# Performance work log

Measured on AMD Instinct MI355X. Metric: run time of the kernel, lower is better.

Reference implementation:

```python
import jax, jax.numpy as jnp
import numpy as np

B, F, D, OUT = 1024, 256, 256, 128
EXP = [10, 25]          # expansion_rates
CUM = [1, 10]           # cum_expansion_rates


def setup_inputs() -> dict:
    key = jax.random.key(0)
    ks = jax.random.split(key, 12)
    s = 0.05
    return {
        "h0": jax.random.normal(ks[0], (B, 1, F), jnp.float32),
        "h1": jax.random.normal(ks[1], (B, EXP[0], F), jnp.float32),
        "h2": jax.random.normal(ks[2], (B, EXP[0] * EXP[1], F), jnp.float32),
        "mask0": (jax.random.uniform(ks[3], (B, 1, EXP[0], 1)) < 0.9).astype(jnp.float32),
        "mask1": (jax.random.uniform(ks[4], (B, EXP[0], EXP[1], 1)) < 0.9).astype(jnp.float32),
        "W_self0": jax.random.normal(ks[5], (D, F), jnp.float32) * s,
        "W_neigh0": jax.random.normal(ks[6], (D, F), jnp.float32) * s,
        "W_pool0": jax.random.normal(ks[7], (D, D), jnp.float32) * s,
        "W_self1": jax.random.normal(ks[8], (D, 2 * D), jnp.float32) * s,
        "W_neigh1": jax.random.normal(ks[9], (D, 2 * D), jnp.float32) * s,
        "W_pool1": jax.random.normal(ks[10], (D, D), jnp.float32) * s,
        "W_out": jax.random.normal(ks[11], (OUT, 2 * D), jnp.float32) * s,
    }


def _sage_layer(x_self, x_neigh, mask, Ws, Wn, Wp):
    # x_self: (B, P, Fin), x_neigh: (B, P, S, Fin), mask: (B, P, S, 1)
    h_self = x_self @ Ws.T                                  # (B, P, D)
    h_neigh = jax.nn.relu(x_neigh @ Wn.T) * mask            # (B, P, S, D)
    h_pool = jnp.max(h_neigh, axis=-2) @ Wp.T               # (B, P, D) -- max pooling
    return jnp.concatenate([h_self, h_pool], axis=-1)       # (B, P, 2D)


def reference(h0, h1, h2, mask0, mask1,
              W_self0, W_neigh0, W_pool0,
              W_self1, W_neigh1, W_pool1, W_out):
    states = [h0, h1, h2]
    masks = [mask0, mask1]
    layers = [(W_self0, W_neigh0, W_pool0), (W_self1, W_neigh1, W_pool1)]
    layer_input_sizes = [F, 2 * D]
    depth = 2
    for i, (Ws, Wn, Wp) in enumerate(layers):
        fin = layer_input_sizes[i]
        for j in range(depth - i):
            x_self = states[j]
            x_neigh = states[j + 1].reshape(-1, CUM[j], EXP[j], fin)
            m = masks[j].reshape(-1, CUM[j], EXP[j], 1)
            states[j] = _sage_layer(x_self, x_neigh, m, Ws, Wn, Wp)
    return states[0][:, 0] @ W_out.T  # (B, OUT)
```

## Files before the change

### kernel.cpp

```cpp
#include <hip/hip_runtime.h>
#include <hip/hip_bf16.h>


typedef __bf16 bf16_t;
typedef bf16_t bf16x8 __attribute__((ext_vector_type(8)));
typedef float  f32x4  __attribute__((ext_vector_type(4)));

__device__ inline bf16x8 cvt8(const float4 a, const float4 b) {
  bf16x8 t;
  t[0]=(bf16_t)a.x; t[1]=(bf16_t)a.y; t[2]=(bf16_t)a.z; t[3]=(bf16_t)a.w;
  t[4]=(bf16_t)b.x; t[5]=(bf16_t)b.y; t[6]=(bf16_t)b.z; t[7]=(bf16_t)b.w;
  return t;
}

__global__ __launch_bounds__(256) void cvt_bf16(
    const float* __restrict__ s, bf16_t* __restrict__ d, int n) {
  const int i = (blockIdx.x * 256 + threadIdx.x) * 8;
  if (i < n) {
    const float4 a = *(const float4*)(s + i);
    const float4 b = *(const float4*)(s + i + 4);
    *(bf16x8*)(d + i) = cvt8(a, b);
  }
}

template<typename AT> struct PreA {
  float4 lo, hi;
  __device__ void fetch(const AT* p) { lo = *(const float4*)p; hi = *(const float4*)(p + 4); }
  __device__ bf16x8 get() const { return cvt8(lo, hi); }
};
template<> struct PreA<bf16_t> {
  bf16x8 v;
  __device__ void fetch(const bf16_t* p) { v = *(const bf16x8*)p; }
  __device__ bf16x8 get() const { return v; }
};

template<int S, int PR, int P, typename AT>
__global__ __launch_bounds__(256) void pool_mfma(
    const AT* __restrict__ A, const bf16_t* __restrict__ W,
    const float* __restrict__ mask, bf16_t* __restrict__ out, int K)
{
  constexpr int ROWS = P * PR;
  constexpr int PM   = ROWS / 16;
  constexpr int MTP  = PR / 16;
  constexpr int APT  = (ROWS * 4) / 256;
  __shared__ bf16x8 Blds[1024];
  __shared__ bf16x8 Alds[ROWS * 4];
  __shared__ float  mlds[P * PR];

  const int tid  = threadIdx.x;
  const int lane = tid & 63, wv = tid >> 6, quad = lane >> 4, lrow = lane & 15;
  const long p0 = (long)blockIdx.x * P;

  if (tid < P * S) mlds[(tid / S) * PR + (tid % S)] = mask[p0 * S + tid];

  const bf16_t* bptr[4];
#pragma unroll
  for (int j = 0; j < 4; ++j) {
    const int s = tid + j * 256;
    bptr[j] = W + (long)((s >> 6) * 16 + (s & 15)) * K + ((s >> 4) & 3) * 8;
  }
  const AT* aptr[APT];
#pragma unroll
  for (int j = 0; j < APT; ++j) {
    const int s  = tid + j * 256;
    const int mr = (s >> 6) * 16 + (s & 15);
    const int p = mr / PR, r = mr % PR;
    const long grow = (p0 + p) * (long)S + (r < S ? r : S - 1);
    aptr[j] = A + grow * (long)K + ((s >> 4) & 3) * 8;
  }

  f32x4 acc[PM][4];
#pragma unroll
  for (int pm = 0; pm < PM; ++pm)
#pragma unroll
    for (int nl = 0; nl < 4; ++nl) acc[pm][nl] = (f32x4){0.f, 0.f, 0.f, 0.f};

  bf16x8 bpre[4];
  PreA<AT> apre[APT];
#pragma unroll
  for (int j = 0; j < 4; ++j) bpre[j] = *(const bf16x8*)(bptr[j]);
#pragma unroll
  for (int j = 0; j < APT; ++j) apre[j].fetch(aptr[j]);

  for (int kt = 0; kt < K; kt += 32) {
    __syncthreads();
#pragma unroll
    for (int j = 0; j < 4; ++j) Blds[tid + j * 256] = bpre[j];
#pragma unroll
    for (int j = 0; j < APT; ++j) Alds[tid + j * 256] = apre[j].get();
    __syncthreads();
    if (kt + 32 < K) {
#pragma unroll
      for (int j = 0; j < 4; ++j) bpre[j] = *(const bf16x8*)(bptr[j] + kt + 32);
#pragma unroll
      for (int j = 0; j < APT; ++j) apre[j].fetch(aptr[j] + kt + 32);
    }
    bf16x8 bfr[4];
#pragma unroll
    for (int nl = 0; nl < 4; ++nl)
      bfr[nl] = Blds[((wv * 4 + nl) * 4 + quad) * 16 + lrow];
#pragma unroll
    for (int pm = 0; pm < PM; ++pm) {
      const bf16x8 afr = Alds[(pm * 4 + quad) * 16 + lrow];
#pragma unroll
      for (int nl = 0; nl < 4; ++nl)
        acc[pm][nl] = __builtin_amdgcn_mfma_f32_16x16x32_bf16(
            afr, bfr[nl], acc[pm][nl], 0, 0, 0);
    }
  }

#pragma unroll
  for (int p = 0; p < P; ++p) {
#pragma unroll
    for (int nl = 0; nl < 4; ++nl) {
      float m = 0.f;
#pragma unroll
      for (int mt = 0; mt < MTP; ++mt) {
        const f32x4 v = acc[p * MTP + mt][nl];
#pragma unroll
        for (int reg = 0; reg < 4; ++reg) {
          const int row = mt * 16 + quad * 4 + reg;
          if (row < S)
            m = fmaxf(m, fmaxf(v[reg], 0.f) * mlds[p * PR + row]);
        }
      }
      m = fmaxf(m, __shfl_xor(m, 16));
      m = fmaxf(m, __shfl_xor(m, 32));
      if (lane < 16)
        out[(p0 + p) * 256 + wv * 64 + nl * 16 + lrow] = (bf16_t)m;
    }
  }
}

template<int MT, int N, typename AT, typename OT>
__global__ __launch_bounds__(256) void plain_mfma(
    const AT* __restrict__ A, const bf16_t* __restrict__ W,
    OT* __restrict__ out, int K, int ldc, int col_off)
{
  constexpr int NTW    = N / 64;
  constexpr int BSLOTS = N * 4;
  constexpr int BPT    = BSLOTS / 256;
  constexpr int ASLOTS = MT * 64;
  __shared__ bf16x8 Blds[BSLOTS];
  __shared__ bf16x8 Alds[ASLOTS];

  const int tid  = threadIdx.x;
  const int lane = tid & 63, wv = tid >> 6, quad = lane >> 4, lrow = lane & 15;
  const long r0 = (long)blockIdx.x * (MT * 16);

  const bf16_t* bptr[BPT];
#pragma unroll
  for (int j = 0; j < BPT; ++j) {
    const int s = tid + j * 256;
    bptr[j] = W + (long)((s >> 6) * 16 + (s & 15)) * K + ((s >> 4) & 3) * 8;
  }
  const bool aact = tid < ASLOTS;
  const AT* aptr = A;
  if (aact) {
    const int mr = (tid >> 6) * 16 + (tid & 15);
    aptr = A + (r0 + mr) * (long)K + ((tid >> 4) & 3) * 8;
  }

  f32x4 acc[MT][NTW];
#pragma unroll
  for (int mt = 0; mt < MT; ++mt)
#pragma unroll
    for (int nl = 0; nl < NTW; ++nl) acc[mt][nl] = (f32x4){0.f, 0.f, 0.f, 0.f};

  bf16x8 bpre[BPT];
  PreA<AT> apre;
#pragma unroll
  for (int j = 0; j < BPT; ++j) bpre[j] = *(const bf16x8*)(bptr[j]);
  if (aact) apre.fetch(aptr);

  for (int kt = 0; kt < K; kt += 32) {
    __syncthreads();
#pragma unroll
    for (int j = 0; j < BPT; ++j) Blds[tid + j * 256] = bpre[j];
    if (aact) Alds[tid] = apre.get();
    __syncthreads();
    if (kt + 32 < K) {
#pragma unroll
      for (int j = 0; j < BPT; ++j) bpre[j] = *(const bf16x8*)(bptr[j] + kt + 32);
      if (aact) apre.fetch(aptr + kt + 32);
    }
    bf16x8 bfr[NTW];
#pragma unroll
    for (int nl = 0; nl < NTW; ++nl)
      bfr[nl] = Blds[((wv * NTW + nl) * 4 + quad) * 16 + lrow];
#pragma unroll
    for (int mt = 0; mt < MT; ++mt) {
      const bf16x8 afr = Alds[(mt * 4 + quad) * 16 + lrow];
#pragma unroll
      for (int nl = 0; nl < NTW; ++nl)
        acc[mt][nl] = __builtin_amdgcn_mfma_f32_16x16x32_bf16(
            afr, bfr[nl], acc[mt][nl], 0, 0, 0);
    }
  }

#pragma unroll
  for (int mt = 0; mt < MT; ++mt)
#pragma unroll
    for (int nl = 0; nl < NTW; ++nl) {
      const f32x4 v = acc[mt][nl];
      const int col = col_off + (wv * NTW + nl) * 16 + lrow;
#pragma unroll
      for (int reg = 0; reg < 4; ++reg) {
        const long row = r0 + mt * 16 + quad * 4 + reg;
        out[row * (long)ldc + col] = (OT)v[reg];
      }
    }
}

extern "C" void kernel_launch(void* const* d_in, const int* in_sizes, int n_in,
                              void* d_out, int out_size, void* d_ws, size_t ws_size,
                              hipStream_t stream) {
  const float* h0    = (const float*)d_in[0];
  const float* h1    = (const float*)d_in[1];
  const float* h2    = (const float*)d_in[2];
  const float* mask0 = (const float*)d_in[3];
  const float* mask1 = (const float*)d_in[4];
  const float* Wf[7] = { (const float*)d_in[5], (const float*)d_in[6],
                         (const float*)d_in[7], (const float*)d_in[8],
                         (const float*)d_in[9], (const float*)d_in[10],
                         (const float*)d_in[11] };
  const int   Wn[7]  = { 65536, 65536, 65536, 131072, 131072, 65536, 65536 };
  float* out = (float*)d_out;

  bf16_t* ws = (bf16_t*)d_ws;
  bf16_t* Wb[7];
  {
    bf16_t* p = ws;
    for (int i = 0; i < 7; ++i) { Wb[i] = p; p += Wn[i]; }
  }
  bf16_t* base = ws + 589824;
  bf16_t* pooled1  = base;
  bf16_t* states1  = pooled1  + 10240L * 256;
  bf16_t* pooled0  = states1  + 10240L * 512;
  bf16_t* states0  = pooled0  + 1024L * 256;
  bf16_t* pooled1b = states0  + 1024L * 512;
  bf16_t* states0b = pooled1b + 1024L * 256;

  const bf16_t *Ws0 = Wb[0], *Wn0 = Wb[1], *Wp0 = Wb[2], *Ws1 = Wb[3],
               *Wn1 = Wb[4], *Wp1 = Wb[5], *Wout = Wb[6];

  const dim3 blk(256);

  for (int i = 0; i < 7; ++i)
    hipLaunchKernelGGL(cvt_bf16, dim3(Wn[i] / 2048), blk, 0, stream,
                       Wf[i], Wb[i], Wn[i]);

  hipLaunchKernelGGL((pool_mfma<25, 32, 4, float>), dim3(2560), blk, 0, stream,
                     h2, Wn0, mask1, pooled1, 256);
  hipLaunchKernelGGL((pool_mfma<10, 16, 8, float>), dim3(128), blk, 0, stream,
                     h1, Wn0, mask0, pooled0, 256);
  hipLaunchKernelGGL((plain_mfma<4, 256, float, bf16_t>), dim3(160), blk, 0, stream,
                     h1, Ws0, states1, 256, 512, 0);
  hipLaunchKernelGGL((plain_mfma<4, 256, bf16_t, bf16_t>), dim3(160), blk, 0, stream,
                     pooled1, Wp0, states1, 256, 512, 256);
  hipLaunchKernelGGL((plain_mfma<1, 256, float, bf16_t>), dim3(64), blk, 0, stream,
                     h0, Ws0, states0, 256, 512, 0);
  hipLaunchKernelGGL((plain_mfma<1, 256, bf16_t, bf16_t>), dim3(64), blk, 0, stream,
                     pooled0, Wp0, states0, 256, 512, 256);
  hipLaunchKernelGGL((pool_mfma<10, 16, 8, bf16_t>), dim3(128), blk, 0, stream,
                     states1, Wn1, mask0, pooled1b, 512);
  hipLaunchKernelGGL((plain_mfma<1, 256, bf16_t, bf16_t>), dim3(64), blk, 0, stream,
                     states0, Ws1, states0b, 512, 512, 0);
  hipLaunchKernelGGL((plain_mfma<1, 256, bf16_t, bf16_t>), dim3(64), blk, 0, stream,
                     pooled1b, Wp1, states0b, 256, 512, 256);
  hipLaunchKernelGGL((plain_mfma<1, 128, bf16_t, float>), dim3(64), blk, 0, stream,
                     states0b, Wout, out, 512, 128, 0);
}
```

Measured before the change: 586.1 us.

## Double-buffer LDS with async global-to-LDS weight loads and merge paired GEMM launches

Weight tiles now go straight into LDS through the global_load_lds builtin, and both operands are double-buffered so each K step needs one barrier instead of two. A register prefetch runs two tiles ahead for the A operand. K becomes a template constant so the loop fully unrolls. h0 and h1 are converted to bf16 once up front, paired GEMMs share one launch through a second grid dimension, and the pool kernels handle fewer parents per block to give more blocks. The cost is extra LDS use, extra conversion kernels and traffic, and more dependence on how the compiler handles the async loads.

```diff
diff --git a/kernel.cpp b/kernel.cpp
--- a/kernel.cpp
+++ b/kernel.cpp
@@ -1,5 +1,4 @@
 #include <hip/hip_runtime.h>
-#include <hip/hip_bf16.h>
 
 
 typedef __bf16 bf16_t;
@@ -21,6 +20,12 @@
     const float4 b = *(const float4*)(s + i + 4);
     *(bf16x8*)(d + i) = cvt8(a, b);
   }
+}
+
+__device__ inline void gload_lds16(const bf16_t* g, bf16x8* l) {
+  __builtin_amdgcn_global_load_lds(
+      (const __attribute__((address_space(1))) unsigned int*)g,
+      (__attribute__((address_space(3))) unsigned int*)l, 16, 0, 0);
 }
 
 template<typename AT> struct PreA {
@@ -34,40 +39,37 @@
   __device__ bf16x8 get() const { return v; }
 };
 
-template<int S, int PR, int P, typename AT>
+template<int S, int PR, int P, int K, typename AT>
 __global__ __launch_bounds__(256) void pool_mfma(
     const AT* __restrict__ A, const bf16_t* __restrict__ W,
-    const float* __restrict__ mask, bf16_t* __restrict__ out, int K)
+    const float* __restrict__ mask, bf16_t* __restrict__ out)
 {
   constexpr int ROWS = P * PR;
   constexpr int PM   = ROWS / 16;
   constexpr int MTP  = PR / 16;
-  constexpr int APT  = (ROWS * 4) / 256;
-  __shared__ bf16x8 Blds[1024];
-  __shared__ bf16x8 Alds[ROWS * 4];
-  __shared__ float  mlds[P * PR];
+  constexpr int T    = K / 32;
+  __shared__ bf16x8 Blds[2][1024];
+  __shared__ bf16x8 Alds[2][ROWS * 4];
+  __shared__ float  mlds[ROWS];
 
   const int tid  = threadIdx.x;
   const int lane = tid & 63, wv = tid >> 6, quad = lane >> 4, lrow = lane & 15;
-  const long p0 = (long)blockIdx.x * P;
+  const long p0  = (long)blockIdx.x * P;
 
   if (tid < P * S) mlds[(tid / S) * PR + (tid % S)] = mask[p0 * S + tid];
 
-  const bf16_t* bptr[4];
+  const bf16_t* wptr[4];
 #pragma unroll
   for (int j = 0; j < 4; ++j) {
-    const int s = tid + j * 256;
-    bptr[j] = W + (long)((s >> 6) * 16 + (s & 15)) * K + ((s >> 4) & 3) * 8;
-  }
-  const AT* aptr[APT];
-#pragma unroll
-  for (int j = 0; j < APT; ++j) {
-    const int s  = tid + j * 256;
-    const int mr = (s >> 6) * 16 + (s & 15);
-    const int p = mr / PR, r = mr % PR;
-    const long grow = (p0 + p) * (long)S + (r < S ? r : S - 1);
-    aptr[j] = A + grow * (long)K + ((s >> 4) & 3) * 8;
-  }
+    const int n = ((tid >> 6) + j * 4) * 16 + (tid & 15);
+    wptr[j] = W + (long)n * K + ((tid >> 4) & 3) * 8;
+  }
+  const int wbase = (tid >> 6) * 64;
+
+  const int mr = (tid >> 6) * 16 + (tid & 15);
+  const int pp = mr / PR, rr = mr % PR;
+  const long grow = (p0 + pp) * (long)S + (rr < S ? rr : S - 1);
+  const AT* aptr = A + grow * (long)K + ((tid >> 4) & 3) * 8;
 
   f32x4 acc[PM][4];
 #pragma unroll
@@ -75,37 +77,39 @@
 #pragma unroll
     for (int nl = 0; nl < 4; ++nl) acc[pm][nl] = (f32x4){0.f, 0.f, 0.f, 0.f};
 
-  bf16x8 bpre[4];
-  PreA<AT> apre[APT];
-#pragma unroll
-  for (int j = 0; j < 4; ++j) bpre[j] = *(const bf16x8*)(bptr[j]);
-#pragma unroll
-  for (int j = 0; j < APT; ++j) apre[j].fetch(aptr[j]);
-
-  for (int kt = 0; kt < K; kt += 32) {
-    __syncthreads();
-#pragma unroll
-    for (int j = 0; j < 4; ++j) Blds[tid + j * 256] = bpre[j];
-#pragma unroll
-    for (int j = 0; j < APT; ++j) Alds[tid + j * 256] = apre[j].get();
-    __syncthreads();
-    if (kt + 32 < K) {
-#pragma unroll
-      for (int j = 0; j < 4; ++j) bpre[j] = *(const bf16x8*)(bptr[j] + kt + 32);
-#pragma unroll
-      for (int j = 0; j < APT; ++j) apre[j].fetch(aptr[j] + kt + 32);
+  PreA<AT> a0, apre[2];
+  a0.fetch(aptr);
+#pragma unroll
+  for (int j = 0; j < 4; ++j) gload_lds16(wptr[j], &Blds[0][wbase + j * 256]);
+  apre[0].fetch(aptr + 32);
+  apre[1].fetch(aptr + 64);
+  Alds[0][tid] = a0.get();
+  __syncthreads();
+
+#pragma unroll
+  for (int i = 0; i < T; ++i) {
+    const int cur = i & 1, nxt = cur ^ 1;
+    if (i + 1 < T) {
+#pragma unroll
+      for (int j = 0; j < 4; ++j)
+        gload_lds16(wptr[j] + (i + 1) * 32, &Blds[nxt][wbase + j * 256]);
     }
     bf16x8 bfr[4];
 #pragma unroll
     for (int nl = 0; nl < 4; ++nl)
-      bfr[nl] = Blds[((wv * 4 + nl) * 4 + quad) * 16 + lrow];
+      bfr[nl] = Blds[cur][((wv * 4 + nl) * 4 + quad) * 16 + lrow];
 #pragma unroll
     for (int pm = 0; pm < PM; ++pm) {
-      const bf16x8 afr = Alds[(pm * 4 + quad) * 16 + lrow];
+      const bf16x8 afr = Alds[cur][(pm * 4 + quad) * 16 + lrow];
 #pragma unroll
       for (int nl = 0; nl < 4; ++nl)
         acc[pm][nl] = __builtin_amdgcn_mfma_f32_16x16x32_bf16(
             afr, bfr[nl], acc[pm][nl], 0, 0, 0);
+    }
+    if (i + 1 < T) {
+      Alds[nxt][tid] = apre[i & 1].get();
+      if (i + 3 < T) apre[i & 1].fetch(aptr + (i + 3) * 32);
+      __syncthreads();
     }
   }
 
@@ -132,70 +136,85 @@
   }
 }
 
-template<int MT, int N, typename AT, typename OT>
+template<int MT, int N, int K, typename OT>
 __global__ __launch_bounds__(256) void plain_mfma(
-    const AT* __restrict__ A, const bf16_t* __restrict__ W,
-    OT* __restrict__ out, int K, int ldc, int col_off)
+    const bf16_t* __restrict__ A0, const bf16_t* __restrict__ W0, int c0,
+    const bf16_t* __restrict__ A1, const bf16_t* __restrict__ W1, int c1,
+    OT* __restrict__ out, int ldc)
 {
   constexpr int NTW    = N / 64;
   constexpr int BSLOTS = N * 4;
   constexpr int BPT    = BSLOTS / 256;
-  constexpr int ASLOTS = MT * 64;
-  __shared__ bf16x8 Blds[BSLOTS];
-  __shared__ bf16x8 Alds[ASLOTS];
+  constexpr int ROWS   = MT * 16;
+  constexpr int ASLOTS = ROWS * 4;
+  constexpr int T      = K / 32;
+  __shared__ bf16x8 Blds[2][BSLOTS];
+  __shared__ bf16x8 Alds[2][ASLOTS];
+
+  const bf16_t* __restrict__ A = blockIdx.y ? A1 : A0;
+  const bf16_t* __restrict__ W = blockIdx.y ? W1 : W0;
+  const int coff = blockIdx.y ? c1 : c0;
 
   const int tid  = threadIdx.x;
   const int lane = tid & 63, wv = tid >> 6, quad = lane >> 4, lrow = lane & 15;
-  const long r0 = (long)blockIdx.x * (MT * 16);
-
-  const bf16_t* bptr[BPT];
+  const long r0  = (long)blockIdx.x * ROWS;
+
+  const bf16_t* wptr[BPT];
 #pragma unroll
   for (int j = 0; j < BPT; ++j) {
-    const int s = tid + j * 256;
-    bptr[j] = W + (long)((s >> 6) * 16 + (s & 15)) * K + ((s >> 4) & 3) * 8;
-  }
+    const int n = ((tid >> 6) + j * 4) * 16 + (tid & 15);
+    wptr[j] = W + (long)n * K + ((tid >> 4) & 3) * 8;
+  }
+  const int wbase = (tid >> 6) * 64;
+
   const bool aact = tid < ASLOTS;
-  const AT* aptr = A;
+  const int  mr   = (tid >> 6) * 16 + (tid & 15);
+  const bf16_t* aptr = A + (aact ? (r0 + mr) * (long)K + ((tid >> 4) & 3) * 8 : 0);
+
+  f32x4 acc[MT][NTW];
+#pragma unroll
+  for (int mt = 0; mt < MT; ++mt)
+#pragma unroll
+    for (int nl = 0; nl < NTW; ++nl) acc[mt][nl] = (f32x4){0.f, 0.f, 0.f, 0.f};
+
+  PreA<bf16_t> a0p, apre[2];
+  if (aact) a0p.fetch(aptr);
+#pragma unroll
+  for (int j = 0; j < BPT; ++j) gload_lds16(wptr[j], &Blds[0][wbase + j * 256]);
   if (aact) {
-    const int mr = (tid >> 6) * 16 + (tid & 15);
-    aptr = A + (r0 + mr) * (long)K + ((tid >> 4) & 3) * 8;
-  }
-
-  f32x4 acc[MT][NTW];
-#pragma unroll
-  for (int mt = 0; mt < MT; ++mt)
-#pragma unroll
-    for (int nl = 0; nl < NTW; ++nl) acc[mt][nl] = (f32x4){0.f, 0.f, 0.f, 0.f};
-
-  bf16x8 bpre[BPT];
-  PreA<AT> apre;
-#pragma unroll
-  for (int j = 0; j < BPT; ++j) bpre[j] = *(const bf16x8*)(bptr[j]);
-  if (aact) apre.fetch(aptr);
-
-  for (int kt = 0; kt < K; kt += 32) {
-    __syncthreads();
-#pragma unroll
-    for (int j = 0; j < BPT; ++j) Blds[tid + j * 256] = bpre[j];
-    if (aact) Alds[tid] = apre.get();
-    __syncthreads();
-    if (kt + 32 < K) {
-#pragma unroll
-      for (int j = 0; j < BPT; ++j) bpre[j] = *(const bf16x8*)(bptr[j] + kt + 32);
-      if (aact) apre.fetch(aptr + kt + 32);
+    apre[0].fetch(aptr + 32);
+    apre[1].fetch(aptr + 64);
+    Alds[0][tid] = a0p.get();
+  }
+  __syncthreads();
+
+#pragma unroll
+  for (int i = 0; i < T; ++i) {
+    const int cur = i & 1, nxt = cur ^ 1;
+    if (i + 1 < T) {
+#pragma unroll
+      for (int j = 0; j < BPT; ++j)
+        gload_lds16(wptr[j] + (i + 1) * 32, &Blds[nxt][wbase + j * 256]);
     }
     bf16x8 bfr[NTW];
 #pragma unroll
     for (int nl = 0; nl < NTW; ++nl)
-      bfr[nl] = Blds[((wv * NTW + nl) * 4 + quad) * 16 + lrow];
+      bfr[nl] = Blds[cur][((wv * NTW + nl) * 4 + quad) * 16 + lrow];
 #pragma unroll
     for (int mt = 0; mt < MT; ++mt) {
-      const bf16x8 afr = Alds[(mt * 4 + quad) * 16 + lrow];
+      const bf16x8 afr = Alds[cur][(mt * 4 + quad) * 16 + lrow];
 #pragma unroll
       for (int nl = 0; nl < NTW; ++nl)
         acc[mt][nl] = __builtin_amdgcn_mfma_f32_16x16x32_bf16(
             afr, bfr[nl], acc[mt][nl], 0, 0, 0);
     }
+    if (i + 1 < T) {
+      if (aact) {
+        Alds[nxt][tid] = apre[i & 1].get();
+        if (i + 3 < T) apre[i & 1].fetch(aptr + (i + 3) * 32);
+      }
+      __syncthreads();
+    }
   }
 
 #pragma unroll
@@ -203,7 +222,7 @@
 #pragma unroll
     for (int nl = 0; nl < NTW; ++nl) {
       const f32x4 v = acc[mt][nl];
-      const int col = col_off + (wv * NTW + nl) * 16 + lrow;
+      const int col = coff + (wv * NTW + nl) * 16 + lrow;
 #pragma unroll
       for (int reg = 0; reg < 4; ++reg) {
         const long row = r0 + mt * 16 + quad * 4 + reg;
@@ -215,8 +234,8 @@
 extern "C" void kernel_launch(void* const* d_in, const int* in_sizes, int n_in,
                               void* d_out, int out_size, void* d_ws, size_t ws_size,
                               hipStream_t stream) {
-  const float* h0    = (const float*)d_in[0];
-  const float* h1    = (const float*)d_in[1];
+  const float* h0f   = (const float*)d_in[0];
+  const float* h1f   = (const float*)d_in[1];
   const float* h2    = (const float*)d_in[2];
   const float* mask0 = (const float*)d_in[3];
   const float* mask1 = (const float*)d_in[4];
@@ -227,47 +246,41 @@
   const int   Wn[7]  = { 65536, 65536, 65536, 131072, 131072, 65536, 65536 };
   float* out = (float*)d_out;
 
-  bf16_t* ws = (bf16_t*)d_ws;
+  bf16_t* p = (bf16_t*)d_ws;
   bf16_t* Wb[7];
-  {
-    bf16_t* p = ws;
-    for (int i = 0; i < 7; ++i) { Wb[i] = p; p += Wn[i]; }
-  }
-  bf16_t* base = ws + 589824;
-  bf16_t* pooled1  = base;
-  bf16_t* states1  = pooled1  + 10240L * 256;
-  bf16_t* pooled0  = states1  + 10240L * 512;
-  bf16_t* states0  = pooled0  + 1024L * 256;
-  bf16_t* pooled1b = states0  + 1024L * 512;
-  bf16_t* states0b = pooled1b + 1024L * 256;
+  for (int i = 0; i < 7; ++i) { Wb[i] = p; p += Wn[i]; }
+  bf16_t* h0b = p;      p += 262144;
+  bf16_t* h1b = p;      p += 2621440;
+  bf16_t* pooled1  = p; p += 10240L * 256;
+  bf16_t* states1  = p; p += 10240L * 512;
+  bf16_t* pooled0  = p; p += 1024L * 256;
+  bf16_t* states0  = p; p += 1024L * 512;
+  bf16_t* pooled1b = p; p += 1024L * 256;
+  bf16_t* states0b = p; p += 1024L * 512;
 
   const bf16_t *Ws0 = Wb[0], *Wn0 = Wb[1], *Wp0 = Wb[2], *Ws1 = Wb[3],
                *Wn1 = Wb[4], *Wp1 = Wb[5], *Wout = Wb[6];
-
   const dim3 blk(256);
 
   for (int i = 0; i < 7; ++i)
-    hipLaunchKernelGGL(cvt_bf16, dim3(Wn[i] / 2048), blk, 0, stream,
-                       Wf[i], Wb[i], Wn[i]);
-
-  hipLaunchKernelGGL((pool_mfma<25, 32, 4, float>), dim3(2560), blk, 0, stream,
-                     h2, Wn0, mask1, pooled1, 256);
-  hipLaunchKernelGGL((pool_mfma<10, 16, 8, float>), dim3(128), blk, 0, stream,
-                     h1, Wn0, mask0, pooled0, 256);
-  hipLaunchKernelGGL((plain_mfma<4, 256, float, bf16_t>), dim3(160), blk, 0, stream,
-                     h1, Ws0, states1, 256, 512, 0);
-  hipLaunchKernelGGL((plain_mfma<4, 256, bf16_t, bf16_t>), dim3(160), blk, 0, stream,
-                     pooled1, Wp0, states1, 256, 512, 256);
-  hipLaunchKernelGGL((plain_mfma<1, 256, float, bf16_t>), dim3(64), blk, 0, stream,
-                     h0, Ws0, states0, 256, 512, 0);
-  hipLaunchKernelGGL((plain_mfma<1, 256, bf16_t, bf16_t>), dim3(64), blk, 0, stream,
-                     pooled0, Wp0, states0, 256, 512, 256);
-  hipLaunchKernelGGL((pool_mfma<10, 16, 8, bf16_t>), dim3(128), blk, 0, stream,
-                     states1, Wn1, mask0, pooled1b, 512);
-  hipLaunchKernelGGL((plain_mfma<1, 256, bf16_t, bf16_t>), dim3(64), blk, 0, stream,
-                     states0, Ws1, states0b, 512, 512, 0);
-  hipLaunchKernelGGL((plain_mfma<1, 256, bf16_t, bf16_t>), dim3(64), blk, 0, stream,
-                     pooled1b, Wp1, states0b, 256, 512, 256);
-  hipLaunchKernelGGL((plain_mfma<1, 128, bf16_t, float>), dim3(64), blk, 0, stream,
-                     states0b, Wout, out, 512, 128, 0);
-}
+    hipLaunchKernelGGL(cvt_bf16, dim3(Wn[i] / 2048), blk, 0, stream, Wf[i], Wb[i], Wn[i]);
+  hipLaunchKernelGGL(cvt_bf16, dim3(128),  blk, 0, stream, h0f, h0b, 262144);
+  hipLaunchKernelGGL(cvt_bf16, dim3(1280), blk, 0, stream, h1f, h1b, 2621440);
+
+  hipLaunchKernelGGL((pool_mfma<25, 32, 2, 256, float>), dim3(5120), blk, 0, stream,
+                     h2, Wn0, mask1, pooled1);
+  hipLaunchKernelGGL((pool_mfma<10, 16, 4, 256, bf16_t>), dim3(256), blk, 0, stream,
+                     h1b, Wn0, mask0, pooled0);
+  hipLaunchKernelGGL((plain_mfma<4, 256, 256, bf16_t>), dim3(160, 2), blk, 0, stream,
+                     h1b, Ws0, 0, pooled1, Wp0, 256, states1, 512);
+  hipLaunchKernelGGL((plain_mfma<1, 256, 256, bf16_t>), dim3(64, 2), blk, 0, stream,
+                     h0b, Ws0, 0, pooled0, Wp0, 256, states0, 512);
+  hipLaunchKernelGGL((pool_mfma<10, 16, 4, 512, bf16_t>), dim3(256), blk, 0, stream,
+                     states1, Wn1, mask0, pooled1b);
+  hipLaunchKernelGGL((plain_mfma<1, 256, 512, bf16_t>), dim3(64, 1), blk, 0, stream,
+                     states0, Ws1, 0, states0, Ws1, 0, states0b, 512);
+  hipLaunchKernelGGL((plain_mfma<1, 256, 256, bf16_t>), dim3(64, 1), blk, 0, stream,
+                     pooled1b, Wp1, 256, pooled1b, Wp1, 256, states0b, 512);
+  hipLaunchKernelGGL((plain_mfma<1, 128, 512, float>), dim3(64, 1), blk, 0, stream,
+                     states0b, Wout, 0, states0b, Wout, 0, out, 128);
+}
```

Measured after the change: 539.4 us. 1.09x faster.
